# Kernel tuning notes

Measured on AMD Instinct MI355X. Metric: run time of the kernel, lower is better.

The kernel has to match this reference:

```python
import jax, jax.numpy as jnp
import numpy as np

N_NODES = 100000
N_EDGES = 3200000
NUM_GRAPHS = 128
IN_DIM = 15
HID = 64


def setup_inputs() -> dict:
    key = jax.random.key(0)
    ks = jax.random.split(key, 12)
    x = jax.random.normal(ks[0], (N_NODES, IN_DIM), dtype=jnp.float32)
    edge_index = jax.random.randint(ks[1], (2, N_EDGES), 0, N_NODES, dtype=jnp.int64)
    batch = jnp.sort(jax.random.randint(ks[2], (N_NODES,), 0, NUM_GRAPHS, dtype=jnp.int64))
    # Glorot-style weights for the 4 GCNConv layers, zero biases (PyG default)
    def glorot(k, fan_in, fan_out):
        s = jnp.sqrt(6.0 / (fan_in + fan_out))
        return jax.random.uniform(k, (fan_in, fan_out), jnp.float32, -s, s)
    return {
        "x": x,
        "w1": glorot(ks[3], IN_DIM, HID), "b1": jnp.zeros((HID,), jnp.float32),
        "w2": glorot(ks[4], HID, HID),    "b2": jnp.zeros((HID,), jnp.float32),
        "w3": glorot(ks[5], HID, HID),    "b3": jnp.zeros((HID,), jnp.float32),
        "w4": glorot(ks[6], HID, HID),    "b4": jnp.zeros((HID,), jnp.float32),
        "edge_index": edge_index,
        "batch": batch,
    }


def _gcn_norm(edge_index, num_nodes):
    # PyG gcn_norm with add_self_loops=True: A_hat = A + I, norm = d^-1/2[src] * d^-1/2[dst]
    loops = jnp.arange(num_nodes, dtype=edge_index.dtype)
    src = jnp.concatenate([edge_index[0], loops])
    dst = jnp.concatenate([edge_index[1], loops])
    deg = jax.ops.segment_sum(jnp.ones_like(dst, dtype=jnp.float32), dst,
                              num_segments=num_nodes)
    dis = jnp.where(deg > 0, jax.lax.rsqrt(deg), 0.0)
    norm = dis[src] * dis[dst]  # [E + N]
    return src, dst, norm


def _gcn_conv(h, w, b, src, dst, norm, num_nodes):
    h = h @ w                               # linear transform first (PyG order)
    msg = h[src] * norm[:, None]            # gather + scale  [E+N, HID]
    agg = jax.ops.segment_sum(msg, dst, num_segments=num_nodes)  # scatter-add
    return agg + b


def reference(x, w1, b1, w2, b2, w3, b3, w4, b4, edge_index, batch):
    n = x.shape[0]
    src, dst, norm = _gcn_norm(edge_index, n)
    h = jax.nn.relu(_gcn_conv(x, w1, b1, src, dst, norm, n))
    h = jax.nn.relu(_gcn_conv(h, w2, b2, src, dst, norm, n))
    h = jax.nn.relu(_gcn_conv(h, w3, b3, src, dst, norm, n))
    h = jax.nn.relu(_gcn_conv(h, w4, b4, src, dst, norm, n))
    # global_mean_pool over graph ids
    sums = jax.ops.segment_sum(h, batch, num_segments=NUM_GRAPHS)
    cnts = jax.ops.segment_sum(jnp.ones((n,), jnp.float32), batch,
                               num_segments=NUM_GRAPHS)
    return sums / jnp.maximum(cnts, 1.0)[:, None]
```

## Files before the change

kernel.cpp:

```cpp
#include <hip/hip_runtime.h>
#include <hip/hip_fp16.h>

#define NN 100000
#define NE 3200000
#define NG 128
#define HID 64

#define BSH 9
#define BNODES 512
#define NBK ((NN + BNODES - 1) / BNODES)
#define CCH 4096

typedef __attribute__((ext_vector_type(2))) _Float16 half2v;
typedef __attribute__((ext_vector_type(4))) _Float16 half4v;

#if __has_builtin(__builtin_amdgcn_fdot2)
#define FDOT2(v, o, a) __builtin_amdgcn_fdot2((v), (o), (a), false)
#else
static __device__ inline float FDOT2(half2v v, half2v o, float a) {
    return a + (float)v.x * (float)o.x + (float)v.y * (float)o.y;
}
#endif

__global__ __launch_bounds__(256) void bcount_kernel(const int* __restrict__ dst,
                                                     int* __restrict__ bcnt, int E) {
    __shared__ int h[NBK];
    for (int i = threadIdx.x; i < NBK; i += 256) h[i] = 0;
    __syncthreads();
    for (int e = blockIdx.x * 256 + threadIdx.x; e < E; e += gridDim.x * 256)
        atomicAdd(&h[dst[e] >> BSH], 1);
    __syncthreads();
    for (int i = threadIdx.x; i < NBK; i += 256)
        if (h[i]) atomicAdd(&bcnt[i], h[i]);
}

__global__ __launch_bounds__(256) void bscan_kernel(const int* __restrict__ bcnt,
                                                    int* __restrict__ bbase,
                                                    int* __restrict__ bcur, int E) {
    __shared__ int s[NBK];
    int t = threadIdx.x;
    if (t < NBK) s[t] = bcnt[t];
    __syncthreads();
    if (t == 0) {
        int acc = 0;
        for (int i = 0; i < NBK; ++i) { int v = s[i]; s[i] = acc; acc += v; }
    }
    __syncthreads();
    if (t < NBK) { bbase[t] = s[t]; bcur[t] = s[t]; }
    if (t == 0) bbase[NBK] = E;
}

__global__ __launch_bounds__(256) void bscatter_kernel(const int* __restrict__ src,
                                                       const int* __restrict__ dst,
                                                       int* __restrict__ bcur,
                                                       unsigned* __restrict__ pairs,
                                                       int E) {
    __shared__ unsigned stage[CCH];
    __shared__ unsigned char bb[CCH];
    __shared__ int cnt[NBK];
    __shared__ int base[NBK];
    const int e0 = blockIdx.x * CCH;
    const int n  = min(CCH, E - e0);
    if (n <= 0) return;
    for (int i = threadIdx.x; i < NBK; i += 256) cnt[i] = 0;
    __syncthreads();
    for (int i = threadIdx.x; i < n; i += 256) {
        int s = src[e0 + i], d = dst[e0 + i];
        int b = d >> BSH;
        stage[i] = ((unsigned)(d & (BNODES - 1)) << 17) | (unsigned)s;
        bb[i] = (unsigned char)b;
        atomicAdd(&cnt[b], 1);
    }
    __syncthreads();
    for (int i = threadIdx.x; i < NBK; i += 256) {
        int c = cnt[i];
        base[i] = c ? atomicAdd(&bcur[i], c) : 0;
        cnt[i] = 0;
    }
    __syncthreads();
    for (int i = threadIdx.x; i < n; i += 256) {
        int b = bb[i];
        int pos = base[b] + atomicAdd(&cnt[b], 1);
        pairs[pos] = stage[i];
    }
}

__global__ __launch_bounds__(256) void csr_kernel(const unsigned* __restrict__ pairs,
                                                  const int* __restrict__ bbase,
                                                  int* __restrict__ rowptr,
                                                  int* __restrict__ csr_src,
                                                  float* __restrict__ dis,
                                                  int N, int E) {
    __shared__ int hist[BNODES];
    __shared__ int cur[BNODES];
    __shared__ int s[256];
    const int b     = blockIdx.x;
    const int t     = threadIdx.x;
    const int node0 = b << BSH;
    const int nn    = min(BNODES, N - node0);
    const int p0 = bbase[b], p1 = bbase[b + 1];

    for (int i = t; i < BNODES; i += 256) hist[i] = 0;
    __syncthreads();
    for (int i = p0 + t; i < p1; i += 256)
        atomicAdd(&hist[pairs[i] >> 17], 1);
    __syncthreads();

    int h0 = hist[2 * t], h1 = hist[2 * t + 1];
    int v = h0 + h1;
    s[t] = v;
    __syncthreads();
    for (int off = 1; off < 256; off <<= 1) {
        int u = (t >= off) ? s[t - off] : 0;
        __syncthreads();
        s[t] += u;
        __syncthreads();
    }
    int excl = s[t] - v;
    int e0 = p0 + excl;
    int e1 = e0 + h0;
    if (2 * t < nn) {
        rowptr[node0 + 2 * t] = e0;
        dis[node0 + 2 * t] = rsqrtf((float)h0 + 1.0f);
        cur[2 * t] = e0;
    }
    if (2 * t + 1 < nn) {
        rowptr[node0 + 2 * t + 1] = e1;
        dis[node0 + 2 * t + 1] = rsqrtf((float)h1 + 1.0f);
        cur[2 * t + 1] = e1;
    }
    if (b == NBK - 1 && t == 0) rowptr[N] = E;
    __syncthreads();

    for (int i = p0 + t; i < p1; i += 256) {
        unsigned p = pairs[i];
        int pos = atomicAdd(&cur[p >> 17], 1);
        csr_src[pos] = (int)(p & 0x1FFFFu);
    }
}

__global__ __launch_bounds__(256) void xprep_kernel(const float* __restrict__ x,
                                                    const float* __restrict__ dis,
                                                    __half* __restrict__ x16h, int N) {
    int gid = blockIdx.x * 256 + threadIdx.x;
    if (gid >= N * 16) return;
    int node = gid >> 4, k = gid & 15;
    float v = (k < 15) ? x[node * 15 + k] * dis[node] : 0.0f;
    x16h[gid] = __float2half(v);
}

__global__ __launch_bounds__(256) void gather16_kernel(const half4v* __restrict__ xh,
                                                       const int* __restrict__ csr_src,
                                                       const int* __restrict__ rowptr,
                                                       const float* __restrict__ dis,
                                                       float4* __restrict__ aggx, int N) {
    const int gid  = blockIdx.x * 256 + threadIdx.x;
    const int node = gid >> 2;
    if (node >= N) return;
    const int l  = threadIdx.x & 3;
    const int gb = threadIdx.x & 60;
    const int start = rowptr[node], end = rowptr[node + 1];
    const half2v ONEX = {(_Float16)1.0f, (_Float16)0.0f};
    const half2v ONEY = {(_Float16)0.0f, (_Float16)1.0f};
    float a0 = 0.0f, a1 = 0.0f, a2 = 0.0f, a3 = 0.0f;
    for (int j0 = start; j0 < end; j0 += 4) {
        int j   = j0 + l;
        int s   = (j < end) ? csr_src[j] : 0;
        int cnt = min(4, end - j0);
#pragma unroll
        for (int k = 0; k < 4; ++k) {
            int sk = __shfl(s, gb + k);
            if (k < cnt) {
                half4v v = xh[sk * 4 + l];
                half2v p0 = __builtin_shufflevector(v, v, 0, 1);
                half2v p1 = __builtin_shufflevector(v, v, 2, 3);
                a0 = FDOT2(p0, ONEX, a0);
                a1 = FDOT2(p0, ONEY, a1);
                a2 = FDOT2(p1, ONEX, a2);
                a3 = FDOT2(p1, ONEY, a3);
            }
        }
    }
    half4v sv = xh[node * 4 + l];
    half2v s0 = __builtin_shufflevector(sv, sv, 0, 1);
    half2v s1 = __builtin_shufflevector(sv, sv, 2, 3);
    a0 += (float)s0.x; a1 += (float)s0.y;
    a2 += (float)s1.x; a3 += (float)s1.y;
    float sn = dis[node];
    aggx[(size_t)node * 4 + l] = make_float4(sn * a0, sn * a1, sn * a2, sn * a3);
}

__global__ __launch_bounds__(256) void gemm12_kernel(const float* __restrict__ in,
                                                     const float* __restrict__ w1,
                                                     const float* __restrict__ b1,
                                                     const float* __restrict__ w2,
                                                     const float* __restrict__ dis,
                                                     __half* __restrict__ th_out, int N) {
    __shared__ float w1_s[16 * 64];
    __shared__ float in_s[64 * 17];
    __shared__ float w2_s[64 * 64];
    __shared__ float h_s[64 * 65];
    const int tid  = threadIdx.x;
    const int row0 = blockIdx.x * 64;
    const int rows = min(64, N - row0);

    for (int i = tid; i < 16 * 64; i += 256) w1_s[i] = (i < 15 * 64) ? w1[i] : 0.0f;
    for (int i = tid; i < 64 * 64; i += 256) w2_s[i] = w2[i];
    for (int i = tid; i < rows * 16; i += 256) {
        int r = i >> 4, k = i & 15;
        in_s[r * 17 + k] = in[(size_t)(row0 + r) * 16 + k];
    }
    __syncthreads();

    const int r  = tid & 63;
    const int cg = tid >> 6;
    {
        float acc[16];
#pragma unroll
        for (int i = 0; i < 16; ++i) acc[i] = 0.0f;
#pragma unroll
        for (int k = 0; k < 16; ++k) {
            float a = in_s[r * 17 + k];
#pragma unroll
            for (int cc = 0; cc < 16; ++cc)
                acc[cc] += a * w1_s[k * 64 + cg * 16 + cc];
        }
#pragma unroll
        for (int cc = 0; cc < 16; ++cc)
            h_s[r * 65 + cg * 16 + cc] = fmaxf(acc[cc] + b1[cg * 16 + cc], 0.0f);
    }
    __syncthreads();
    {
        const float2* w2v = reinterpret_cast<const float2*>(w2_s);
        float2 acc2[8];
#pragma unroll
        for (int i = 0; i < 8; ++i) acc2[i] = make_float2(0.0f, 0.0f);
#pragma unroll
        for (int k = 0; k < 64; ++k) {
            float a = h_s[r * 65 + k];
            const float2* wk = w2v + k * 32 + cg * 8;
#pragma unroll
            for (int i = 0; i < 8; ++i) {
                float2 wv = wk[i];
                acc2[i].x += a * wv.x;
                acc2[i].y += a * wv.y;
            }
        }
        const int row = row0 + r;
        if (row < N) {
            float sd = dis[row];
            __align__(16) __half2 hh[8];
#pragma unroll
            for (int i = 0; i < 8; ++i)
                hh[i] = __floats2half2_rn(acc2[i].x * sd, acc2[i].y * sd);
            float4* tp = reinterpret_cast<float4*>(th_out + (size_t)row * HID + cg * 16);
            tp[0] = reinterpret_cast<float4*>(hh)[0];
            tp[1] = reinterpret_cast<float4*>(hh)[1];
        }
    }
}

__global__ __launch_bounds__(256) void gatherRB_kernel(const half2v* __restrict__ th,
                                                       const int* __restrict__ csr_src,
                                                       const int* __restrict__ rowptr,
                                                       const float* __restrict__ dis,
                                                       const float* __restrict__ bias,
                                                       __half* __restrict__ U, int N) {
    const int gid  = blockIdx.x * 256 + threadIdx.x;
    const int node = gid >> 5;
    if (node >= N) return;
    const int l  = threadIdx.x & 31;
    const int hb = threadIdx.x & 32;
    const int start = rowptr[node], end = rowptr[node + 1];
    const half2v* tl = th + l;
    const half2v ONEX = {(_Float16)1.0f, (_Float16)0.0f};
    const half2v ONEY = {(_Float16)0.0f, (_Float16)1.0f};
    float ax = 0.0f, ay = 0.0f;
    for (int j0 = start; j0 < end; j0 += 32) {
        int j   = j0 + l;
        int s   = (j < end) ? csr_src[j] : 0;
        int cnt = min(32, end - j0);
        int k = 0;
        for (; k + 16 <= cnt; k += 16) {
            int sk[16];
#pragma unroll
            for (int u = 0; u < 16; ++u) sk[u] = __shfl(s, hb + k + u);
            half2v v[16];
#pragma unroll
            for (int u = 0; u < 16; ++u) v[u] = tl[sk[u] * 32];
#pragma unroll
            for (int u = 0; u < 16; ++u) {
                ax = FDOT2(v[u], ONEX, ax);
                ay = FDOT2(v[u], ONEY, ay);
            }
        }
        for (; k + 4 <= cnt; k += 4) {
            int s0 = __shfl(s, hb + k);
            int s1 = __shfl(s, hb + k + 1);
            int s2 = __shfl(s, hb + k + 2);
            int s3 = __shfl(s, hb + k + 3);
            half2v v0 = tl[s0 * 32];
            half2v v1 = tl[s1 * 32];
            half2v v2 = tl[s2 * 32];
            half2v v3 = tl[s3 * 32];
            ax = FDOT2(v0, ONEX, ax); ay = FDOT2(v0, ONEY, ay);
            ax = FDOT2(v1, ONEX, ax); ay = FDOT2(v1, ONEY, ay);
            ax = FDOT2(v2, ONEX, ax); ay = FDOT2(v2, ONEY, ay);
            ax = FDOT2(v3, ONEX, ax); ay = FDOT2(v3, ONEY, ay);
        }
        for (; k < cnt; ++k) {
            half2v v = tl[__shfl(s, hb + k) * 32];
            ax += (float)v.x; ay += (float)v.y;
        }
    }
    half2v self = tl[node * 32];
    ax += (float)self.x; ay += (float)self.y;
    float sn = dis[node];
    float2 bv = reinterpret_cast<const float2*>(bias)[l];
    float u0 = fmaxf(sn * ax + bv.x, 0.0f);
    float u1 = fmaxf(sn * ay + bv.y, 0.0f);
    reinterpret_cast<__half2*>(U)[(size_t)node * 32 + l] = __floats2half2_rn(u0, u1);
}

__global__ __launch_bounds__(256) void gemmH_kernel(const __half2* __restrict__ Uh,
                                                    const float* __restrict__ w,
                                                    const float* __restrict__ dis,
                                                    __half* __restrict__ th_out, int N) {
    __shared__ float w_s[64 * 64];
    __shared__ float in_s[64 * 65];
    const int tid  = threadIdx.x;
    const int row0 = blockIdx.x * 64;
    const int rows = min(64, N - row0);

    for (int i = tid; i < 64 * 64; i += 256) w_s[i] = w[i];
    for (int i = tid; i < rows * 32; i += 256) {
        int r = i >> 5, kp = i & 31;
        float2 v = __half22float2(Uh[(size_t)(row0 + r) * 32 + kp]);
        in_s[r * 65 + 2 * kp]     = v.x;
        in_s[r * 65 + 2 * kp + 1] = v.y;
    }
    __syncthreads();

    const int r  = tid & 63;
    const int cg = tid >> 6;
    const float2* wv = reinterpret_cast<const float2*>(w_s);
    float2 acc2[8];
#pragma unroll
    for (int i = 0; i < 8; ++i) acc2[i] = make_float2(0.0f, 0.0f);
#pragma unroll
    for (int k = 0; k < 64; ++k) {
        float a = in_s[r * 65 + k];
        const float2* wk = wv + k * 32 + cg * 8;
#pragma unroll
        for (int i = 0; i < 8; ++i) {
            float2 ww = wk[i];
            acc2[i].x += a * ww.x;
            acc2[i].y += a * ww.y;
        }
    }
    const int row = row0 + r;
    if (row < N) {
        float sd = dis[row];
        __align__(16) __half2 hh[8];
#pragma unroll
        for (int i = 0; i < 8; ++i)
            hh[i] = __floats2half2_rn(acc2[i].x * sd, acc2[i].y * sd);
        float4* tp = reinterpret_cast<float4*>(th_out + (size_t)row * HID + cg * 16);
        tp[0] = reinterpret_cast<float4*>(hh)[0];
        tp[1] = reinterpret_cast<float4*>(hh)[1];
    }
}

__global__ __launch_bounds__(256) void poolH_kernel(const __half* __restrict__ U,
                                                    const int* __restrict__ batch,
                                                    float* __restrict__ sums,
                                                    float* __restrict__ cnts, int N) {
    __shared__ float lsum[NG * HID];
    __shared__ float lcnt[NG];
    const int tid  = threadIdx.x;
    const int base = blockIdx.x * 256;
    const int last = min(base + 256, N) - 1;
    const int gfirst = batch[base];
    const int glast  = batch[last];
    const int span   = glast - gfirst + 1;

    for (int i = tid; i < span * HID; i += 256) lsum[i] = 0.0f;
    for (int i = tid; i < span; i += 256) lcnt[i] = 0.0f;
    __syncthreads();

    const int f = tid & 63, sub = tid >> 6;
    for (int n = base + sub; n < min(base + 256, N); n += 4) {
        int g = batch[n];
        float v = __half2float(U[(size_t)n * HID + f]);
        atomicAdd(&lsum[(g - gfirst) * HID + f], v);
        if (f == 0) atomicAdd(&lcnt[g - gfirst], 1.0f);
    }
    __syncthreads();

    for (int i = tid; i < span * HID; i += 256)
        atomicAdd(&sums[(size_t)gfirst * HID + i], lsum[i]);
    for (int i = tid; i < span; i += 256) atomicAdd(&cnts[gfirst + i], lcnt[i]);
}

__global__ __launch_bounds__(256) void finalize_kernel(const float* __restrict__ sums,
                                                       const float* __restrict__ cnts,
                                                       float* __restrict__ out) {
    int i = blockIdx.x * 256 + threadIdx.x;
    if (i < NG * HID) out[i] = sums[i] / fmaxf(cnts[i >> 6], 1.0f);
}

extern "C" void kernel_launch(void* const* d_in, const int* in_sizes, int n_in,
                              void* d_out, int out_size, void* d_ws, size_t ws_size,
                              hipStream_t stream) {
    const float* x  = (const float*)d_in[0];
    const float* w1 = (const float*)d_in[1];
    const float* b1 = (const float*)d_in[2];
    const float* w2 = (const float*)d_in[3];
    const float* b2 = (const float*)d_in[4];
    const float* w3 = (const float*)d_in[5];
    const float* b3 = (const float*)d_in[6];
    const float* w4 = (const float*)d_in[7];
    const float* b4 = (const float*)d_in[8];
    const int* ei    = (const int*)d_in[9];
    const int* batch = (const int*)d_in[10];
    const int* src = ei;
    const int* dst = ei + NE;

    __half*   thA     = (__half*)d_ws;
    __half*   thB     = thA + (size_t)NN * HID;
    __half*   U       = thB + (size_t)NN * HID;
    unsigned* pairs   = (unsigned*)(U + (size_t)NN * HID);
    float*    aggx    = (float*)pairs;
    __half*   x16h    = (__half*)(aggx + (size_t)NN * 16);
    int*      csr_src = (int*)((char*)pairs + (size_t)NE * 4);
    int*      rowptr  = csr_src + NE;
    float*    dis     = (float*)(rowptr + NN + 1);
    int*      bcnt    = (int*)(dis + NN);
    int*      bbase   = bcnt + NBK;
    int*      bcur    = bbase + NBK + 1;
    float*    sums    = (float*)(bcur + NBK);
    float*    cnts    = sums + NG * HID;

    float* out = (float*)d_out;

    const int NB  = (NN + 255) / 256;
    const int GB  = (NN + 63) / 64;
    const int XB  = (NN * 16 + 255) / 256;
    const int OB  = (NN * 4 + 255) / 256;
    const int HB  = (NN * 32 + 255) / 256;
    const int CB  = (NE + CCH - 1) / CCH;

    hipMemsetAsync(bcnt, 0, NBK * sizeof(int), stream);
    hipMemsetAsync(sums, 0, (NG * HID + NG) * sizeof(float), stream);

    bcount_kernel<<<512, 256, 0, stream>>>(dst, bcnt, NE);
    bscan_kernel<<<1, 256, 0, stream>>>(bcnt, bbase, bcur, NE);
    bscatter_kernel<<<CB, 256, 0, stream>>>(src, dst, bcur, pairs, NE);
    csr_kernel<<<NBK, 256, 0, stream>>>(pairs, bbase, rowptr, csr_src, dis, NN, NE);

    xprep_kernel<<<XB, 256, 0, stream>>>(x, dis, x16h, NN);
    gather16_kernel<<<OB, 256, 0, stream>>>((const half4v*)x16h, csr_src, rowptr, dis,
                                            (float4*)aggx, NN);
    gemm12_kernel<<<GB, 256, 0, stream>>>(aggx, w1, b1, w2, dis, thA, NN);
    gatherRB_kernel<<<HB, 256, 0, stream>>>((const half2v*)thA, csr_src, rowptr, dis,
                                            b2, U, NN);
    gemmH_kernel<<<GB, 256, 0, stream>>>((const __half2*)U, w3, dis, thB, NN);
    gatherRB_kernel<<<HB, 256, 0, stream>>>((const half2v*)thB, csr_src, rowptr, dis,
                                            b3, U, NN);
    gemmH_kernel<<<GB, 256, 0, stream>>>((const __half2*)U, w4, dis, thA, NN);
    gatherRB_kernel<<<HB, 256, 0, stream>>>((const half2v*)thA, csr_src, rowptr, dis,
                                            b4, U, NN);
    poolH_kernel<<<NB, 256, 0, stream>>>(U, batch, sums, cnts, NN);
    finalize_kernel<<<(NG * HID + 255) / 256, 256, 0, stream>>>(sums, cnts, out);
}
```

Before: 549.4 us.

## Split hidden features into four column-quarter planes for the gather kernels

Stores the 64-wide fp16 hidden features as four separate planes of 16 features per node, in both the GEMM outputs and the gather outputs. The gather kernel now gives each node 8 lanes covering one quarter, and the block index is mapped so the blocks working on each plane run close together in time. This shrinks the working set each gather touches at once (100K nodes × 32 B per plane) so it fits better in L2/MALL, trading full 128 B row gathers for four 32 B gathers per edge. The edge index list is read four times, the loops are shorter (8 edges per chunk), and the pooling and GEMM kernels now read strided plane addresses.

```diff
diff --git a/kernel.cpp b/kernel.cpp
--- a/kernel.cpp
+++ b/kernel.cpp
@@ -195,7 +195,7 @@
                                                      const float* __restrict__ b1,
                                                      const float* __restrict__ w2,
                                                      const float* __restrict__ dis,
-                                                     __half* __restrict__ th_out, int N) {
+                                                     __half* __restrict__ thq, int N) {
     __shared__ float w1_s[16 * 64];
     __shared__ float in_s[64 * 17];
     __shared__ float w2_s[64 * 64];
@@ -253,79 +253,68 @@
 #pragma unroll
             for (int i = 0; i < 8; ++i)
                 hh[i] = __floats2half2_rn(acc2[i].x * sd, acc2[i].y * sd);
-            float4* tp = reinterpret_cast<float4*>(th_out + (size_t)row * HID + cg * 16);
+            float4* tp = reinterpret_cast<float4*>(thq + ((size_t)cg * N + row) * 16);
             tp[0] = reinterpret_cast<float4*>(hh)[0];
             tp[1] = reinterpret_cast<float4*>(hh)[1];
         }
     }
 }
 
-__global__ __launch_bounds__(256) void gatherRB_kernel(const half2v* __restrict__ th,
-                                                       const int* __restrict__ csr_src,
-                                                       const int* __restrict__ rowptr,
-                                                       const float* __restrict__ dis,
-                                                       const float* __restrict__ bias,
-                                                       __half* __restrict__ U, int N) {
-    const int gid  = blockIdx.x * 256 + threadIdx.x;
-    const int node = gid >> 5;
+__global__ __launch_bounds__(256) void gatherQ_kernel(const half2v* __restrict__ thq,
+                                                      const int* __restrict__ csr_src,
+                                                      const int* __restrict__ rowptr,
+                                                      const float* __restrict__ dis,
+                                                      const float* __restrict__ bias,
+                                                      __half2* __restrict__ Uq, int N) {
+    const int b     = blockIdx.x;
+    const int q     = (b & 7) >> 1;
+    const int node0 = (b >> 3) * 64 + (b & 1) * 32;
+    const int l     = threadIdx.x & 7;
+    const int slot  = threadIdx.x >> 3;
+    const int node  = node0 + slot;
     if (node >= N) return;
-    const int l  = threadIdx.x & 31;
-    const int hb = threadIdx.x & 32;
+    const int gb = (threadIdx.x & 63) & 56;
     const int start = rowptr[node], end = rowptr[node + 1];
-    const half2v* tl = th + l;
+    const half2v* tl = thq + (size_t)q * N * 8 + l;
     const half2v ONEX = {(_Float16)1.0f, (_Float16)0.0f};
     const half2v ONEY = {(_Float16)0.0f, (_Float16)1.0f};
     float ax = 0.0f, ay = 0.0f;
-    for (int j0 = start; j0 < end; j0 += 32) {
+    for (int j0 = start; j0 < end; j0 += 8) {
         int j   = j0 + l;
         int s   = (j < end) ? csr_src[j] : 0;
-        int cnt = min(32, end - j0);
-        int k = 0;
-        for (; k + 16 <= cnt; k += 16) {
-            int sk[16];
-#pragma unroll
-            for (int u = 0; u < 16; ++u) sk[u] = __shfl(s, hb + k + u);
-            half2v v[16];
-#pragma unroll
-            for (int u = 0; u < 16; ++u) v[u] = tl[sk[u] * 32];
-#pragma unroll
-            for (int u = 0; u < 16; ++u) {
+        int cnt = min(8, end - j0);
+        if (cnt == 8) {
+            int sk[8];
+#pragma unroll
+            for (int u = 0; u < 8; ++u) sk[u] = __shfl(s, gb + u);
+            half2v v[8];
+#pragma unroll
+            for (int u = 0; u < 8; ++u) v[u] = tl[(size_t)sk[u] * 8];
+#pragma unroll
+            for (int u = 0; u < 8; ++u) {
                 ax = FDOT2(v[u], ONEX, ax);
                 ay = FDOT2(v[u], ONEY, ay);
             }
-        }
-        for (; k + 4 <= cnt; k += 4) {
-            int s0 = __shfl(s, hb + k);
-            int s1 = __shfl(s, hb + k + 1);
-            int s2 = __shfl(s, hb + k + 2);
-            int s3 = __shfl(s, hb + k + 3);
-            half2v v0 = tl[s0 * 32];
-            half2v v1 = tl[s1 * 32];
-            half2v v2 = tl[s2 * 32];
-            half2v v3 = tl[s3 * 32];
-            ax = FDOT2(v0, ONEX, ax); ay = FDOT2(v0, ONEY, ay);
-            ax = FDOT2(v1, ONEX, ax); ay = FDOT2(v1, ONEY, ay);
-            ax = FDOT2(v2, ONEX, ax); ay = FDOT2(v2, ONEY, ay);
-            ax = FDOT2(v3, ONEX, ax); ay = FDOT2(v3, ONEY, ay);
-        }
-        for (; k < cnt; ++k) {
-            half2v v = tl[__shfl(s, hb + k) * 32];
-            ax += (float)v.x; ay += (float)v.y;
-        }
-    }
-    half2v self = tl[node * 32];
+        } else {
+            for (int k = 0; k < cnt; ++k) {
+                half2v v = tl[(size_t)__shfl(s, gb + k) * 8];
+                ax += (float)v.x; ay += (float)v.y;
+            }
+        }
+    }
+    half2v self = tl[(size_t)node * 8];
     ax += (float)self.x; ay += (float)self.y;
     float sn = dis[node];
-    float2 bv = reinterpret_cast<const float2*>(bias)[l];
+    float2 bv = reinterpret_cast<const float2*>(bias)[q * 8 + l];
     float u0 = fmaxf(sn * ax + bv.x, 0.0f);
     float u1 = fmaxf(sn * ay + bv.y, 0.0f);
-    reinterpret_cast<__half2*>(U)[(size_t)node * 32 + l] = __floats2half2_rn(u0, u1);
-}
-
-__global__ __launch_bounds__(256) void gemmH_kernel(const __half2* __restrict__ Uh,
-                                                    const float* __restrict__ w,
-                                                    const float* __restrict__ dis,
-                                                    __half* __restrict__ th_out, int N) {
+    Uq[(size_t)q * N * 8 + (size_t)node * 8 + l] = __floats2half2_rn(u0, u1);
+}
+
+__global__ __launch_bounds__(256) void gemmHQ_kernel(const __half2* __restrict__ Uq,
+                                                     const float* __restrict__ w,
+                                                     const float* __restrict__ dis,
+                                                     __half* __restrict__ thq, int N) {
     __shared__ float w_s[64 * 64];
     __shared__ float in_s[64 * 65];
     const int tid  = threadIdx.x;
@@ -335,7 +324,8 @@
     for (int i = tid; i < 64 * 64; i += 256) w_s[i] = w[i];
     for (int i = tid; i < rows * 32; i += 256) {
         int r = i >> 5, kp = i & 31;
-        float2 v = __half22float2(Uh[(size_t)(row0 + r) * 32 + kp]);
+        int q = kp >> 3, lp = kp & 7;
+        float2 v = __half22float2(Uq[((size_t)q * N + row0 + r) * 8 + lp]);
         in_s[r * 65 + 2 * kp]     = v.x;
         in_s[r * 65 + 2 * kp + 1] = v.y;
     }
@@ -365,16 +355,16 @@
 #pragma unroll
         for (int i = 0; i < 8; ++i)
             hh[i] = __floats2half2_rn(acc2[i].x * sd, acc2[i].y * sd);
-        float4* tp = reinterpret_cast<float4*>(th_out + (size_t)row * HID + cg * 16);
+        float4* tp = reinterpret_cast<float4*>(thq + ((size_t)cg * N + row) * 16);
         tp[0] = reinterpret_cast<float4*>(hh)[0];
         tp[1] = reinterpret_cast<float4*>(hh)[1];
     }
 }
 
-__global__ __launch_bounds__(256) void poolH_kernel(const __half* __restrict__ U,
-                                                    const int* __restrict__ batch,
-                                                    float* __restrict__ sums,
-                                                    float* __restrict__ cnts, int N) {
+__global__ __launch_bounds__(256) void poolHQ_kernel(const __half* __restrict__ Uq,
+                                                     const int* __restrict__ batch,
+                                                     float* __restrict__ sums,
+                                                     float* __restrict__ cnts, int N) {
     __shared__ float lsum[NG * HID];
     __shared__ float lcnt[NG];
     const int tid  = threadIdx.x;
@@ -389,9 +379,10 @@
     __syncthreads();
 
     const int f = tid & 63, sub = tid >> 6;
+    const int q = f >> 4, j = f & 15;
     for (int n = base + sub; n < min(base + 256, N); n += 4) {
         int g = batch[n];
-        float v = __half2float(U[(size_t)n * HID + f]);
+        float v = __half2float(Uq[((size_t)q * N + n) * 16 + j]);
         atomicAdd(&lsum[(g - gfirst) * HID + f], v);
         if (f == 0) atomicAdd(&lcnt[g - gfirst], 1.0f);
     }
@@ -428,8 +419,8 @@
 
     __half*   thA     = (__half*)d_ws;
     __half*   thB     = thA + (size_t)NN * HID;
-    __half*   U       = thB + (size_t)NN * HID;
-    unsigned* pairs   = (unsigned*)(U + (size_t)NN * HID);
+    __half*   Uq      = thB + (size_t)NN * HID;
+    unsigned* pairs   = (unsigned*)(Uq + (size_t)NN * HID);
     float*    aggx    = (float*)pairs;
     __half*   x16h    = (__half*)(aggx + (size_t)NN * 16);
     int*      csr_src = (int*)((char*)pairs + (size_t)NE * 4);
@@ -447,7 +438,7 @@
     const int GB  = (NN + 63) / 64;
     const int XB  = (NN * 16 + 255) / 256;
     const int OB  = (NN * 4 + 255) / 256;
-    const int HB  = (NN * 32 + 255) / 256;
+    const int GQ  = ((NN + 63) / 64) * 8;
     const int CB  = (NE + CCH - 1) / CCH;
 
     hipMemsetAsync(bcnt, 0, NBK * sizeof(int), stream);
@@ -462,14 +453,14 @@
     gather16_kernel<<<OB, 256, 0, stream>>>((const half4v*)x16h, csr_src, rowptr, dis,
                                             (float4*)aggx, NN);
     gemm12_kernel<<<GB, 256, 0, stream>>>(aggx, w1, b1, w2, dis, thA, NN);
-    gatherRB_kernel<<<HB, 256, 0, stream>>>((const half2v*)thA, csr_src, rowptr, dis,
-                                            b2, U, NN);
-    gemmH_kernel<<<GB, 256, 0, stream>>>((const __half2*)U, w3, dis, thB, NN);
-    gatherRB_kernel<<<HB, 256, 0, stream>>>((const half2v*)thB, csr_src, rowptr, dis,
-                                            b3, U, NN);
-    gemmH_kernel<<<GB, 256, 0, stream>>>((const __half2*)U, w4, dis, thA, NN);
-    gatherRB_kernel<<<HB, 256, 0, stream>>>((const half2v*)thA, csr_src, rowptr, dis,
-                                            b4, U, NN);
-    poolH_kernel<<<NB, 256, 0, stream>>>(U, batch, sums, cnts, NN);
+    gatherQ_kernel<<<GQ, 256, 0, stream>>>((const half2v*)thA, csr_src, rowptr, dis,
+                                           b2, (__half2*)Uq, NN);
+    gemmHQ_kernel<<<GB, 256, 0, stream>>>((const __half2*)Uq, w3, dis, thB, NN);
+    gatherQ_kernel<<<GQ, 256, 0, stream>>>((const half2v*)thB, csr_src, rowptr, dis,
+                                           b3, (__half2*)Uq, NN);
+    gemmHQ_kernel<<<GB, 256, 0, stream>>>((const __half2*)Uq, w4, dis, thA, NN);
+    gatherQ_kernel<<<GQ, 256, 0, stream>>>((const half2v*)thA, csr_src, rowptr, dis,
+                                           b4, (__half2*)Uq, NN);
+    poolHQ_kernel<<<NB, 256, 0, stream>>>(Uq, batch, sums, cnts, NN);
     finalize_kernel<<<(NG * HID + 255) / 256, 256, 0, stream>>>(sums, cnts, out);
 }
```

New measurement: 628.3 us. 1.14x slower.
